# Optimization experiments

Measured on AMD Instinct MI355X. Metric: run time of the kernel, lower is better.

Reference implementation:

```python
import jax, jax.numpy as jnp
import numpy as np

B, T, D = 2, 2048, 1024
NH, NKV, HD = 16, 4, 64
ROPE = 16  # partial RoPE dims (first 16 of 64)
HALF = ROPE // 2


def apply_rope(x, cos, sin):
    # x: (B, nH, T, HD); rotate first ROPE dims, pass the rest through
    x1 = x[..., :HALF]
    x2 = x[..., HALF:ROPE]
    xp = x[..., ROPE:]
    c = cos[None, None, :, :]  # (1,1,T,HALF)
    s = sin[None, None, :, :]
    return jnp.concatenate([x1 * c - x2 * s, x1 * s + x2 * c, xp], axis=-1)


def setup_inputs() -> dict:
    key = jax.random.key(0)
    k0, k1, k2 = jax.random.split(key, 3)
    x = jax.random.normal(k0, (B, T, D), dtype=jnp.float32)
    # RoPE tables for the rotated sub-dimension (half = ROPE//2 = 8)
    inv_freq = 1.0 / (10000.0 ** (jnp.arange(HALF, dtype=jnp.float32) / HALF))
    ang = jnp.arange(T, dtype=jnp.float32)[:, None] * inv_freq[None, :]
    cos = jnp.cos(ang)
    sin = jnp.sin(ang)
    attn_mask = jnp.tril(jnp.ones((T, T), dtype=bool))  # causal
    w_qkv = jax.random.normal(k1, ((NH + 2 * NKV) * HD, D), dtype=jnp.float32) * (D ** -0.5)
    w_out = jax.random.normal(k2, (D, D), dtype=jnp.float32) * (D ** -0.5)
    q_scale = jnp.full((NH, 1), 1.5, dtype=jnp.float32)
    k_scale = jnp.full((NKV, 1), 1.5, dtype=jnp.float32)
    return {"x": x, "cos": cos, "sin": sin, "attn_mask": attn_mask,
            "w_qkv": w_qkv, "w_out": w_out, "q_scale": q_scale, "k_scale": k_scale}


def reference(x, cos, sin, attn_mask, w_qkv, w_out, q_scale, k_scale):
    Bx, Tx, C = x.shape
    groups = NH // NKV
    qkv = x @ w_qkv.T  # (B,T,(NH+2*NKV)*HD)
    q, k, v = jnp.split(qkv, [NH * HD, (NH + NKV) * HD], axis=-1)
    q = q.reshape(Bx, Tx, NH, HD).transpose(0, 2, 1, 3)    # (B,NH,T,HD)
    k = k.reshape(Bx, Tx, NKV, HD).transpose(0, 2, 1, 3)   # (B,NKV,T,HD)
    v = v.reshape(Bx, Tx, NKV, HD).transpose(0, 2, 1, 3)
    # per-head qk gain scaling
    q = q * q_scale[None, :, :, None]  # (1,NH,1,1)
    k = k * k_scale[None, :, :, None]
    # partial RoPE on q and k
    q = apply_rope(q, cos[:Tx], sin[:Tx])
    k = apply_rope(k, cos[:Tx], sin[:Tx])
    # GQA expand (repeat_interleave along heads)
    ke = jnp.repeat(k, groups, axis=1)  # (B,NH,T,HD)
    ve = jnp.repeat(v, groups, axis=1)
    # scaled dot-product attention with causal mask
    scores = jnp.einsum('bhqd,bhkd->bhqk', q, ke) * (HD ** -0.5)
    scores = jnp.where(attn_mask[None, None], scores, -jnp.inf)
    probs = jax.nn.softmax(scores, axis=-1)
    ao = jnp.einsum('bhqk,bhkd->bhqd', probs, ve)  # (B,NH,T,HD)
    # xsa: subtract self-component along the (shared) kv value direction
    ao_r = ao.reshape(Bx, NKV, groups, Tx, HD)
    vv = v[:, :, None]  # (B,NKV,1,T,HD), broadcasts over groups
    dots = jnp.sum(ao_r * vv, axis=-1, keepdims=True)
    norm = jnp.maximum(jnp.sum(vv * vv, axis=-1, keepdims=True), 1e-8)
    ao = (ao_r - (dots / norm) * vv).reshape(Bx, NH, Tx, HD)
    out = ao.transpose(0, 2, 1, 3).reshape(Bx, Tx, C) @ w_out.T
    return out
```

## Files before the change

### kernel.cpp

```cpp
#include <hip/hip_runtime.h>
#include <hip/hip_bf16.h>

#define NB 2
#define NT 2048
#define ND 1024
#define NHEADS 16
#define NKVH 4
#define HDIM 64
#define QKVD 1536

typedef __attribute__((ext_vector_type(8))) short short8;
typedef __attribute__((ext_vector_type(4))) float floatx4;

#if defined(__has_builtin)
#  if __has_builtin(__builtin_amdgcn_global_load_lds)
#    define HAS_GLL 1
#  endif
#endif
#ifndef HAS_GLL
#  define HAS_GLL 0
#endif

__device__ __forceinline__ void gll16(const void* g, void* l, int lane) {
#if HAS_GLL
  (void)lane;
  __builtin_amdgcn_global_load_lds(
      (const __attribute__((address_space(1))) unsigned int*)g,
      (__attribute__((address_space(3))) unsigned int*)l, 16, 0, 0);
#else
  *(short8*)((short*)l) = *(const short8*)g;
#endif
}

__device__ __forceinline__ unsigned short f2bf(float f) {
  union { float f; unsigned int u; } cv; cv.f = f;
  unsigned int u = cv.u;
  u += 0x7fffu + ((u >> 16) & 1u);
  return (unsigned short)(u >> 16);
}
__device__ __forceinline__ float bf2f(unsigned short u) {
  union { unsigned int u; float f; } cv; cv.u = ((unsigned int)u) << 16; return cv.f;
}

#define N4_X   1048576
#define N4_WQ   393216
#define N4_WO   262144
__global__ __launch_bounds__(256) void cvt_all(
    const float* __restrict__ x, const float* __restrict__ wq,
    const float* __restrict__ wo,
    unsigned short* __restrict__ xb, unsigned short* __restrict__ wqb,
    unsigned short* __restrict__ wob) {
  int i = blockIdx.x * 256 + threadIdx.x;
  const float* src; unsigned short* dst; int j;
  if (i < N4_X)              { src = x;  dst = xb;  j = i; }
  else if (i < N4_X + N4_WQ) { src = wq; dst = wqb; j = i - N4_X; }
  else                       { src = wo; dst = wob; j = i - N4_X - N4_WQ; }
  float4 v = ((const float4*)src)[j];
  ushort4 o;
  o.x = f2bf(v.x); o.y = f2bf(v.y); o.z = f2bf(v.z); o.w = f2bf(v.w);
  ((ushort4*)dst)[j] = o;
}

#define GEMM4W_PROLOGUE(Aptr, Bptr, Kdim)                                      \
  __shared__ __align__(16) short As[2][128][32];                               \
  __shared__ __align__(16) short Bs[2][128][32];                               \
  const int tid = threadIdx.x;                                                 \
  const int wid = tid >> 6;                                                    \
  const int wr = wid >> 1, wc = wid & 1;                                       \
  const int lane = tid & 63;                                                   \
  const int quad = lane >> 4, l16 = lane & 15;                                 \
  const int srow = tid >> 2;                                                   \
  const int sch  = ((tid & 3) ^ (srow & 3)) * 8;                               \
  const unsigned short* agp = (Aptr) + (size_t)(m0 + srow) * (Kdim) + sch;     \
  const unsigned short* bgp = (Bptr) + (size_t)(n0 + srow) * (Kdim) + sch;     \
  short* asb = &As[0][0][0];                                                   \
  short* bsb = &Bs[0][0][0];                                                   \
  const int lofs = (HAS_GLL ? wid * 512 : tid * 8);                            \
  const int cs = (quad ^ (l16 & 3)) * 8;                                       \
  floatx4 acc[4][4] = {};                                                      \
  _Pragma("unroll")                                                            \
  for (int g = 0; g < 2; g++) {                                                \
    gll16(agp + (size_t)(64 * g) * (Kdim), asb + g * 2048 + lofs, lane);       \
    gll16(bgp + (size_t)(64 * g) * (Kdim), bsb + g * 2048 + lofs, lane);       \
  }                                                                            \
  const int NIT = (Kdim) / 32;                                                 \
  for (int it = 0; it < NIT; it++) {                                           \
    __syncthreads();                                                           \
    const int bi = it & 1, bn = bi ^ 1;                                        \
    if (it + 1 < NIT) {                                                        \
      const int k = (it + 1) * 32;                                             \
      _Pragma("unroll")                                                        \
      for (int g = 0; g < 2; g++) {                                            \
        gll16(agp + (size_t)(64 * g) * (Kdim) + k, asb + bn * 4096 + g * 2048 + lofs, lane); \
        gll16(bgp + (size_t)(64 * g) * (Kdim) + k, bsb + bn * 4096 + g * 2048 + lofs, lane); \
      }                                                                        \
    }                                                                          \
    short8 af[4], bf[4];                                                       \
    _Pragma("unroll")                                                          \
    for (int mi = 0; mi < 4; mi++)                                             \
      af[mi] = *(const short8*)(asb + bi * 4096 + (wr * 64 + mi * 16 + l16) * 32 + cs); \
    _Pragma("unroll")                                                          \
    for (int ni = 0; ni < 4; ni++)                                             \
      bf[ni] = *(const short8*)(bsb + bi * 4096 + (wc * 64 + ni * 16 + l16) * 32 + cs); \
    _Pragma("unroll")                                                          \
    for (int mi = 0; mi < 4; mi++)                                             \
      _Pragma("unroll")                                                        \
      for (int ni = 0; ni < 4; ni++)                                           \
        acc[mi][ni] = __builtin_amdgcn_mfma_f32_16x16x32_bf16(af[mi], bf[ni], acc[mi][ni], 0, 0, 0); \
  }

__global__ __launch_bounds__(256) void gemm_qkv(
    const unsigned short* __restrict__ A,
    const unsigned short* __restrict__ Bm,
    const float* __restrict__ cosT, const float* __restrict__ sinT,
    const float* __restrict__ q_scale, const float* __restrict__ k_scale,
    unsigned short* __restrict__ qb, unsigned short* __restrict__ kb,
    unsigned short* __restrict__ vtb)
{
  const int m0 = blockIdx.x * 128, n0 = blockIdx.y * 128;
  GEMM4W_PROLOGUE(A, Bm, ND)

  const int hh = blockIdx.y * 2 + wc;
  const int mw0 = m0 + wr * 64;
  const int lo8 = l16 & 7;

  if (hh >= NHEADS + NKVH) {
    const int kvh = hh - (NHEADS + NKVH);
#pragma unroll
    for (int mi = 0; mi < 4; mi++) {
      const int mrow = mw0 + mi * 16 + quad * 4;
      const int bb = mrow >> 11, tt = mrow & (NT - 1);
#pragma unroll
      for (int ni = 0; ni < 4; ni++) {
        const int d = ni * 16 + l16;
        ushort4 w;
        w.x = f2bf(acc[mi][ni][0]); w.y = f2bf(acc[mi][ni][1]);
        w.z = f2bf(acc[mi][ni][2]); w.w = f2bf(acc[mi][ni][3]);
        *(ushort4*)(vtb + ((size_t)((bb * NKVH + kvh) * HDIM + d)) * NT + tt) = w;
      }
    }
  } else {
    float scl; unsigned short* dst0; int hloc, nh;
    if (hh < NHEADS) { scl = q_scale[hh] * (0.125f * 1.44269504088896f); hloc = hh; dst0 = qb; nh = NHEADS; }
    else             { scl = k_scale[hh - NHEADS]; hloc = hh - NHEADS; dst0 = kb; nh = NKVH; }
#pragma unroll
    for (int mi = 0; mi < 4; mi++) {
#pragma unroll
      for (int r = 0; r < 4; r++) {
        const int mrow = mw0 + mi * 16 + quad * 4 + r;
        const int bb = mrow >> 11, tt = mrow & (NT - 1);
        unsigned short* drow = dst0 + ((size_t)((bb * nh + hloc) * NT + tt)) * HDIM;

        const float own = acc[mi][0][r];
        const float oth = __shfl_xor(own, 8);
        const float c = cosT[tt * 8 + lo8], s = sinT[tt * 8 + lo8];
        const float roped = (l16 < 8) ? (own * c - oth * s)
                                      : (oth * s + own * c);
        drow[l16] = f2bf(roped * scl);
#pragma unroll
        for (int ni = 1; ni < 4; ni++)
          drow[ni * 16 + l16] = f2bf(acc[mi][ni][r] * scl);
      }
    }
  }
}

__global__ __launch_bounds__(256) void gemm_out(
    const unsigned short* __restrict__ A,
    const unsigned short* __restrict__ Bm,
    float* __restrict__ C, int M, int N, int K)
{
  const int m0 = blockIdx.x * 128, n0 = blockIdx.y * 128;
  GEMM4W_PROLOGUE(A, Bm, K)

#pragma unroll
  for (int mi = 0; mi < 4; mi++)
#pragma unroll
    for (int ni = 0; ni < 4; ni++)
#pragma unroll
      for (int r = 0; r < 4; r++) {
        int m = m0 + wr * 64 + mi * 16 + quad * 4 + r;
        int n = n0 + wc * 64 + ni * 16 + l16;
        C[(size_t)m * N + n] = acc[mi][ni][r];
      }
}

__global__ __launch_bounds__(256) void fattn(
    const unsigned short* __restrict__ qb,
    const unsigned short* __restrict__ kb,
    const unsigned short* __restrict__ vtb,
    unsigned short* __restrict__ aob,
    float* __restrict__ pbuf)
{
  const int idx = blockIdx.x;
  const int h = blockIdx.y, b = blockIdx.z;
  const int kv = h >> 2;

  int qt, j0, cnt, chunk; bool direct;
  if (idx < 16) { qt = 16 + idx; j0 = 0; cnt = 16; chunk = 0; direct = false; }
  else {
    int rel = idx - 16, s = 16 - (rel >> 1);
    if ((rel & 1) == 0) { qt = s - 1;  j0 = 0;  cnt = s; chunk = 0; direct = true;  }
    else                { qt = s + 15; j0 = 16; cnt = s; chunk = 1; direct = false; }
  }

  const int tid = threadIdx.x;
  const int wid = tid >> 6, lane = tid & 63;
  const int quad = lane >> 4, l16 = lane & 15;
  const int lo8 = l16 & 7;

  __shared__ __align__(16) short Ks[2][64][64];
  __shared__ __align__(16) short Vs[2][64][64];
  __shared__ __align__(16) short Ps[4][16][64];

  const unsigned short* qg = qb + ((size_t)((b * NHEADS + h) * NT + qt * 64)) * HDIM;
  const int qrow = wid * 16 + l16;
  short8 aq0 = *(const short8*)(qg + (size_t)qrow * HDIM + quad * 8);
  short8 aq1 = *(const short8*)(qg + (size_t)qrow * HDIM + 32 + quad * 8);

  const int sr  = tid >> 3;
  const int lck = ((tid & 7) ^ (sr & 7)) * 8;
  const unsigned short* kgp0 = kb  + ((size_t)((b * NKVH + kv) * NT) + sr) * HDIM + lck;
  const unsigned short* vgp0 = vtb + ((size_t)((b * NKVH + kv) * HDIM) + sr) * NT + lck;
  short* ksb = &Ks[0][0][0];
  short* vsb = &Vs[0][0][0];
  const int lofs = (HAS_GLL ? wid * 512 : tid * 8);

  const int cs0 = (quad ^ lo8) * 8;
  const int cs1 = cs0 ^ 32;

  char* psb = (char*)&Ps[0][0][0];
  int psw[4];
#pragma unroll
  for (int nb = 0; nb < 4; nb++)
    psw[nb] = wid * 2048 + l16 * 128 +
              ((((nb << 1) | (quad >> 1)) ^ lo8) << 4) + ((quad & 1) << 3);
  const int pr0 = wid * 2048 + l16 * 128 + ((quad ^ lo8) << 4);

  floatx4 acc_o[4] = {};
  float lsum = 0.f;

  {
    const unsigned short* kg = kgp0 + (size_t)j0 * 64 * HDIM;
    const unsigned short* vg = vgp0 + j0 * 64;
    gll16(kg, ksb + lofs, lane);
    gll16(kg + 32 * HDIM, ksb + 2048 + lofs, lane);
    gll16(vg, vsb + lofs, lane);
    gll16(vg + (size_t)32 * NT, vsb + 2048 + lofs, lane);
  }

  for (int i = 0; i < cnt; i++) {
    const int jt = j0 + i;
    __syncthreads();
    const int bi = i & 1, bn = bi ^ 1;
    if (i + 1 < cnt) {
      const unsigned short* kg = kgp0 + (size_t)(jt + 1) * 64 * HDIM;
      const unsigned short* vg = vgp0 + (jt + 1) * 64;
      gll16(kg, ksb + bn * 4096 + lofs, lane);
      gll16(kg + 32 * HDIM, ksb + bn * 4096 + 2048 + lofs, lane);
      gll16(vg, vsb + bn * 4096 + lofs, lane);
      gll16(vg + (size_t)32 * NT, vsb + bn * 4096 + 2048 + lofs, lane);
    }

    floatx4 s[4] = {};
#pragma unroll
    for (int nb = 0; nb < 4; nb++) {
      short8 bk0 = *(const short8*)&Ks[bi][nb * 16 + l16][cs0];
      short8 bk1 = *(const short8*)&Ks[bi][nb * 16 + l16][cs1];
      s[nb] = __builtin_amdgcn_mfma_f32_16x16x32_bf16(bk0, aq0, s[nb], 0, 0, 0);
      s[nb] = __builtin_amdgcn_mfma_f32_16x16x32_bf16(bk1, aq1, s[nb], 0, 0, 0);
    }

    if (jt == qt) {
      const int qloc = wid * 16 + l16;
#pragma unroll
      for (int nb = 0; nb < 4; nb++)
#pragma unroll
        for (int r = 0; r < 4; r++)
          if (nb * 16 + quad * 4 + r > qloc) s[nb][r] = -INFINITY;
    }

#pragma unroll
    for (int nb = 0; nb < 4; nb++) {
      float p0 = __builtin_amdgcn_exp2f(s[nb][0]);
      float p1 = __builtin_amdgcn_exp2f(s[nb][1]);
      float p2 = __builtin_amdgcn_exp2f(s[nb][2]);
      float p3 = __builtin_amdgcn_exp2f(s[nb][3]);
      lsum += (p0 + p1) + (p2 + p3);
      unsigned int pk0, pk1;
      asm("v_cvt_pk_bf16_f32 %0, %1, %2" : "=v"(pk0) : "v"(p0), "v"(p1));
      asm("v_cvt_pk_bf16_f32 %0, %1, %2" : "=v"(pk1) : "v"(p2), "v"(p3));
      uint2 w; w.x = pk0; w.y = pk1;
      *(uint2*)(psb + psw[nb]) = w;
    }

    short8 ap0 = *(const short8*)(psb + pr0);
    short8 ap1 = *(const short8*)(psb + (pr0 ^ 64));
#pragma unroll
    for (int nb = 0; nb < 4; nb++) {
      short8 bv0 = *(const short8*)&Vs[bi][nb * 16 + l16][cs0];
      short8 bv1 = *(const short8*)&Vs[bi][nb * 16 + l16][cs1];
      acc_o[nb] = __builtin_amdgcn_mfma_f32_16x16x32_bf16(ap0, bv0, acc_o[nb], 0, 0, 0);
      acc_o[nb] = __builtin_amdgcn_mfma_f32_16x16x32_bf16(ap1, bv1, acc_o[nb], 0, 0, 0);
    }
  }

  const int bl = (cnt - 1) & 1;

  float lst = lsum;
  lst += __shfl_xor(lst, 16);
  lst += __shfl_xor(lst, 32);

  if (direct) {
#pragma unroll
    for (int r = 0; r < 4; r++) {
      const int rowl = wid * 16 + quad * 4 + r;
      const float invl = 1.f / __shfl(lst, quad * 4 + r);

      const int vcol = ((rowl >> 3) ^ lo8) * 8 + (rowl & 7);
      float vd[4], dot = 0.f, vv = 0.f;
#pragma unroll
      for (int nb = 0; nb < 4; nb++) {
        vd[nb] = bf2f((unsigned short)Vs[bl][nb * 16 + l16][vcol]);
        dot += acc_o[nb][r] * invl * vd[nb];
        vv  += vd[nb] * vd[nb];
      }
#pragma unroll
      for (int off = 1; off < 16; off <<= 1) {
        dot += __shfl_xor(dot, off);
        vv  += __shfl_xor(vv, off);
      }
      const float coef = dot / fmaxf(vv, 1e-8f);
      unsigned short* dst = aob + ((size_t)(b * NT + qt * 64 + rowl)) * ND + h * HDIM + l16;
#pragma unroll
      for (int nb = 0; nb < 4; nb++)
        dst[nb * 16] = f2bf(acc_o[nb][r] * invl - coef * vd[nb]);
    }
  } else {
    const int slot = ((b * NHEADS + h) * 16 + (qt - 16)) * 2 + chunk;
    float* pO = pbuf + (size_t)slot * 4160;
    float* pl = pO + 4096;
    if (quad == 0) pl[wid * 16 + l16] = lst;
#pragma unroll
    for (int r = 0; r < 4; r++) {
      const int rowl = wid * 16 + quad * 4 + r;
#pragma unroll
      for (int nb = 0; nb < 4; nb++)
        pO[rowl * 64 + nb * 16 + l16] = acc_o[nb][r];
    }
  }
}

__global__ __launch_bounds__(256) void redn(
    const float* __restrict__ pbuf,
    const unsigned short* __restrict__ vtb,
    unsigned short* __restrict__ aob)
{
  const int qt = 16 + blockIdx.x;
  const int h = blockIdx.y, b = blockIdx.z;
  const int kv = h >> 2;
  const int tid = threadIdx.x;

  const int slot0 = ((b * NHEADS + h) * 16 + blockIdx.x) * 2;
  const float* O0 = pbuf + (size_t)slot0 * 4160;
  const float* O1 = O0 + 4160;
  const float* l0 = O0 + 4096;
  const float* l1 = O1 + 4096;

  __shared__ short vt[64][66];

  {
    const int d = tid >> 2, tq = (tid & 3) * 16;
    const unsigned short* src = vtb + ((size_t)((b * NKVH + kv) * HDIM + d)) * NT + qt * 64 + tq;
    short8 v0 = *(const short8*)src;
    short8 v1 = *(const short8*)(src + 8);
    *(short8*)&vt[d][tq] = v0;
    *(short8*)&vt[d][tq + 8] = v1;
  }
  __syncthreads();

  const int row = tid >> 2, dq = tid & 3;
  const float invl = 1.f / (l0[row] + l1[row]);

  float o[16], vd[16];
  float dot = 0.f, vv = 0.f;
#pragma unroll
  for (int j = 0; j < 16; j++) {
    const int d = dq * 16 + j;
    float ov = (O0[row * 64 + d] + O1[row * 64 + d]) * invl;
    float v  = bf2f((unsigned short)vt[d][row]);
    o[j] = ov; vd[j] = v;
    dot += ov * v; vv += v * v;
  }
  dot += __shfl_xor(dot, 1); dot += __shfl_xor(dot, 2);
  vv  += __shfl_xor(vv, 1);  vv  += __shfl_xor(vv, 2);
  const float coef = dot / fmaxf(vv, 1e-8f);

  unsigned short* dst = aob + ((size_t)(b * NT + qt * 64 + row)) * ND + h * HDIM + dq * 16;
  ushort4 w0, w1, w2, w3;
  w0.x = f2bf(o[0] - coef * vd[0]);  w0.y = f2bf(o[1] - coef * vd[1]);
  w0.z = f2bf(o[2] - coef * vd[2]);  w0.w = f2bf(o[3] - coef * vd[3]);
  w1.x = f2bf(o[4] - coef * vd[4]);  w1.y = f2bf(o[5] - coef * vd[5]);
  w1.z = f2bf(o[6] - coef * vd[6]);  w1.w = f2bf(o[7] - coef * vd[7]);
  w2.x = f2bf(o[8] - coef * vd[8]);  w2.y = f2bf(o[9] - coef * vd[9]);
  w2.z = f2bf(o[10] - coef * vd[10]); w2.w = f2bf(o[11] - coef * vd[11]);
  w3.x = f2bf(o[12] - coef * vd[12]); w3.y = f2bf(o[13] - coef * vd[13]);
  w3.z = f2bf(o[14] - coef * vd[14]); w3.w = f2bf(o[15] - coef * vd[15]);
  ((ushort4*)dst)[0] = w0; ((ushort4*)dst)[1] = w1;
  ((ushort4*)dst)[2] = w2; ((ushort4*)dst)[3] = w3;
}

extern "C" void kernel_launch(void* const* d_in, const int* in_sizes, int n_in,
                              void* d_out, int out_size, void* d_ws, size_t ws_size,
                              hipStream_t stream) {
  const float* x       = (const float*)d_in[0];
  const float* cosT    = (const float*)d_in[1];
  const float* sinT    = (const float*)d_in[2];
  const float* w_qkv   = (const float*)d_in[4];
  const float* w_out   = (const float*)d_in[5];
  const float* q_scale = (const float*)d_in[6];
  const float* k_scale = (const float*)d_in[7];
  float* out = (float*)d_out;

  char* ws = (char*)d_ws;
  unsigned short* xb    = (unsigned short*)ws;
  unsigned short* wqkvb = (unsigned short*)(ws + 8388608);
  float*          pbuf  = (float*)ws;
  unsigned short* woutb = (unsigned short*)(ws + 17825792);
  unsigned short* qb    = (unsigned short*)(ws + 19922944);
  unsigned short* kb    = (unsigned short*)(ws + 28311552);
  unsigned short* vtb   = (unsigned short*)(ws + 30408704);
  unsigned short* aob   = (unsigned short*)(ws + 32505856);

  cvt_all<<<(N4_X + N4_WQ + N4_WO) / 256, 256, 0, stream>>>(
      x, w_qkv, w_out, xb, wqkvb, woutb);

  gemm_qkv<<<dim3(NB * NT / 128, QKVD / 128), 256, 0, stream>>>(
      xb, wqkvb, cosT, sinT, q_scale, k_scale, qb, kb, vtb);

  fattn<<<dim3(48, NHEADS, NB), 256, 0, stream>>>(qb, kb, vtb, aob, pbuf);
  redn<<<dim3(16, NHEADS, NB), 256, 0, stream>>>(pbuf, vtb, aob);

  gemm_out<<<dim3(NB * NT / 128, ND / 128), 256, 0, stream>>>(
      aob, woutb, out, NB * NT, ND, ND);
}
```

Before: 191.9 us.

## Quadruple-buffer K/V tiles and sync every two attention iterations

The K/V shared-memory staging grows from two to four buffers. The prologue preloads the first two tiles, and the loop now issues prefetches for tiles i+2 and i+3 behind a single barrier taken on even iterations. This halves the number of block barriers and gives async loads more lead time. The cost is doubled K/V LDS usage, which may lower the number of resident blocks per CU.

```diff
diff --git a/kernel.cpp b/kernel.cpp
--- a/kernel.cpp
+++ b/kernel.cpp
@@ -209,8 +209,8 @@
   const int quad = lane >> 4, l16 = lane & 15;
   const int lo8 = l16 & 7;
 
-  __shared__ __align__(16) short Ks[2][64][64];
-  __shared__ __align__(16) short Vs[2][64][64];
+  __shared__ __align__(16) short Ks[4][64][64];
+  __shared__ __align__(16) short Vs[4][64][64];
   __shared__ __align__(16) short Ps[4][16][64];
 
   const unsigned short* qg = qb + ((size_t)((b * NHEADS + h) * NT + qt * 64)) * HDIM;
@@ -247,19 +247,39 @@
     gll16(kg + 32 * HDIM, ksb + 2048 + lofs, lane);
     gll16(vg, vsb + lofs, lane);
     gll16(vg + (size_t)32 * NT, vsb + 2048 + lofs, lane);
+    if (cnt > 1) {
+      const unsigned short* kg1 = kgp0 + (size_t)(j0 + 1) * 64 * HDIM;
+      const unsigned short* vg1 = vgp0 + (j0 + 1) * 64;
+      gll16(kg1, ksb + 4096 + lofs, lane);
+      gll16(kg1 + 32 * HDIM, ksb + 4096 + 2048 + lofs, lane);
+      gll16(vg1, vsb + 4096 + lofs, lane);
+      gll16(vg1 + (size_t)32 * NT, vsb + 4096 + 2048 + lofs, lane);
+    }
   }
 
   for (int i = 0; i < cnt; i++) {
     const int jt = j0 + i;
-    __syncthreads();
-    const int bi = i & 1, bn = bi ^ 1;
-    if (i + 1 < cnt) {
-      const unsigned short* kg = kgp0 + (size_t)(jt + 1) * 64 * HDIM;
-      const unsigned short* vg = vgp0 + (jt + 1) * 64;
-      gll16(kg, ksb + bn * 4096 + lofs, lane);
-      gll16(kg + 32 * HDIM, ksb + bn * 4096 + 2048 + lofs, lane);
-      gll16(vg, vsb + bn * 4096 + lofs, lane);
-      gll16(vg + (size_t)32 * NT, vsb + bn * 4096 + 2048 + lofs, lane);
+    const int bi = i & 3;
+    if ((i & 1) == 0) {
+      __syncthreads();
+      if (i + 2 < cnt) {
+        const int b2 = (i + 2) & 3;
+        const unsigned short* kg = kgp0 + (size_t)(jt + 2) * 64 * HDIM;
+        const unsigned short* vg = vgp0 + (jt + 2) * 64;
+        gll16(kg, ksb + b2 * 4096 + lofs, lane);
+        gll16(kg + 32 * HDIM, ksb + b2 * 4096 + 2048 + lofs, lane);
+        gll16(vg, vsb + b2 * 4096 + lofs, lane);
+        gll16(vg + (size_t)32 * NT, vsb + b2 * 4096 + 2048 + lofs, lane);
+      }
+      if (i + 3 < cnt) {
+        const int b3 = (i + 3) & 3;
+        const unsigned short* kg = kgp0 + (size_t)(jt + 3) * 64 * HDIM;
+        const unsigned short* vg = vgp0 + (jt + 3) * 64;
+        gll16(kg, ksb + b3 * 4096 + lofs, lane);
+        gll16(kg + 32 * HDIM, ksb + b3 * 4096 + 2048 + lofs, lane);
+        gll16(vg, vsb + b3 * 4096 + lofs, lane);
+        gll16(vg + (size_t)32 * NT, vsb + b3 * 4096 + 2048 + lofs, lane);
+      }
     }
 
     floatx4 s[4] = {};
@@ -305,7 +325,7 @@
     }
   }
 
-  const int bl = (cnt - 1) & 1;
+  const int bl = (cnt - 1) & 3;
 
   float lst = lsum;
   lst += __shfl_xor(lst, 16);
```

New measurement: 199.3 us. 3.9% more time.

## Drop split-KV attention and reduction kernel; one block per query tile, longest first

Applied to the files above, without the earlier changes.

Replaces the split-KV scheme, which split the upper query tiles into two chunks with a float partial buffer and a separate reduction kernel, with a plain one-block-per-query-tile causal attention launch. Tiles are ordered heaviest first to balance the triangular workload. This removes the partial-buffer round trip and one kernel launch. In exchange the per-block work becomes more uneven (up to 32 KV tiles) and there are fewer blocks, which can lengthen the tail.

```diff
diff --git a/kernel.cpp b/kernel.cpp
--- a/kernel.cpp
+++ b/kernel.cpp
@@ -189,20 +189,12 @@
     const unsigned short* __restrict__ qb,
     const unsigned short* __restrict__ kb,
     const unsigned short* __restrict__ vtb,
-    unsigned short* __restrict__ aob,
-    float* __restrict__ pbuf)
+    unsigned short* __restrict__ aob)
 {
-  const int idx = blockIdx.x;
+  const int qt = (NT / 64 - 1) - blockIdx.x;
   const int h = blockIdx.y, b = blockIdx.z;
   const int kv = h >> 2;
-
-  int qt, j0, cnt, chunk; bool direct;
-  if (idx < 16) { qt = 16 + idx; j0 = 0; cnt = 16; chunk = 0; direct = false; }
-  else {
-    int rel = idx - 16, s = 16 - (rel >> 1);
-    if ((rel & 1) == 0) { qt = s - 1;  j0 = 0;  cnt = s; chunk = 0; direct = true;  }
-    else                { qt = s + 15; j0 = 16; cnt = s; chunk = 1; direct = false; }
-  }
+  const int cnt = qt + 1;
 
   const int tid = threadIdx.x;
   const int wid = tid >> 6, lane = tid & 63;
@@ -241,8 +233,8 @@
   float lsum = 0.f;
 
   {
-    const unsigned short* kg = kgp0 + (size_t)j0 * 64 * HDIM;
-    const unsigned short* vg = vgp0 + j0 * 64;
+    const unsigned short* kg = kgp0;
+    const unsigned short* vg = vgp0;
     gll16(kg, ksb + lofs, lane);
     gll16(kg + 32 * HDIM, ksb + 2048 + lofs, lane);
     gll16(vg, vsb + lofs, lane);
@@ -250,7 +242,7 @@
   }
 
   for (int i = 0; i < cnt; i++) {
-    const int jt = j0 + i;
+    const int jt = i;
     __syncthreads();
     const int bi = i & 1, bn = bi ^ 1;
     if (i + 1 < cnt) {
@@ -311,103 +303,30 @@
   lst += __shfl_xor(lst, 16);
   lst += __shfl_xor(lst, 32);
 
-  if (direct) {
-#pragma unroll
-    for (int r = 0; r < 4; r++) {
-      const int rowl = wid * 16 + quad * 4 + r;
-      const float invl = 1.f / __shfl(lst, quad * 4 + r);
-
-      const int vcol = ((rowl >> 3) ^ lo8) * 8 + (rowl & 7);
-      float vd[4], dot = 0.f, vv = 0.f;
-#pragma unroll
-      for (int nb = 0; nb < 4; nb++) {
-        vd[nb] = bf2f((unsigned short)Vs[bl][nb * 16 + l16][vcol]);
-        dot += acc_o[nb][r] * invl * vd[nb];
-        vv  += vd[nb] * vd[nb];
-      }
-#pragma unroll
-      for (int off = 1; off < 16; off <<= 1) {
-        dot += __shfl_xor(dot, off);
-        vv  += __shfl_xor(vv, off);
-      }
-      const float coef = dot / fmaxf(vv, 1e-8f);
-      unsigned short* dst = aob + ((size_t)(b * NT + qt * 64 + rowl)) * ND + h * HDIM + l16;
-#pragma unroll
-      for (int nb = 0; nb < 4; nb++)
-        dst[nb * 16] = f2bf(acc_o[nb][r] * invl - coef * vd[nb]);
-    }
-  } else {
-    const int slot = ((b * NHEADS + h) * 16 + (qt - 16)) * 2 + chunk;
-    float* pO = pbuf + (size_t)slot * 4160;
-    float* pl = pO + 4096;
-    if (quad == 0) pl[wid * 16 + l16] = lst;
-#pragma unroll
-    for (int r = 0; r < 4; r++) {
-      const int rowl = wid * 16 + quad * 4 + r;
-#pragma unroll
-      for (int nb = 0; nb < 4; nb++)
-        pO[rowl * 64 + nb * 16 + l16] = acc_o[nb][r];
-    }
-  }
-}
-
-__global__ __launch_bounds__(256) void redn(
-    const float* __restrict__ pbuf,
-    const unsigned short* __restrict__ vtb,
-    unsigned short* __restrict__ aob)
-{
-  const int qt = 16 + blockIdx.x;
-  const int h = blockIdx.y, b = blockIdx.z;
-  const int kv = h >> 2;
-  const int tid = threadIdx.x;
-
-  const int slot0 = ((b * NHEADS + h) * 16 + blockIdx.x) * 2;
-  const float* O0 = pbuf + (size_t)slot0 * 4160;
-  const float* O1 = O0 + 4160;
-  const float* l0 = O0 + 4096;
-  const float* l1 = O1 + 4096;
-
-  __shared__ short vt[64][66];
-
-  {
-    const int d = tid >> 2, tq = (tid & 3) * 16;
-    const unsigned short* src = vtb + ((size_t)((b * NKVH + kv) * HDIM + d)) * NT + qt * 64 + tq;
-    short8 v0 = *(const short8*)src;
-    short8 v1 = *(const short8*)(src + 8);
-    *(short8*)&vt[d][tq] = v0;
-    *(short8*)&vt[d][tq + 8] = v1;
-  }
-  __syncthreads();
-
-  const int row = tid >> 2, dq = tid & 3;
-  const float invl = 1.f / (l0[row] + l1[row]);
-
-  float o[16], vd[16];
-  float dot = 0.f, vv = 0.f;
-#pragma unroll
-  for (int j = 0; j < 16; j++) {
-    const int d = dq * 16 + j;
-    float ov = (O0[row * 64 + d] + O1[row * 64 + d]) * invl;
-    float v  = bf2f((unsigned short)vt[d][row]);
-    o[j] = ov; vd[j] = v;
-    dot += ov * v; vv += v * v;
-  }
-  dot += __shfl_xor(dot, 1); dot += __shfl_xor(dot, 2);
-  vv  += __shfl_xor(vv, 1);  vv  += __shfl_xor(vv, 2);
-  const float coef = dot / fmaxf(vv, 1e-8f);
-
-  unsigned short* dst = aob + ((size_t)(b * NT + qt * 64 + row)) * ND + h * HDIM + dq * 16;
-  ushort4 w0, w1, w2, w3;
-  w0.x = f2bf(o[0] - coef * vd[0]);  w0.y = f2bf(o[1] - coef * vd[1]);
-  w0.z = f2bf(o[2] - coef * vd[2]);  w0.w = f2bf(o[3] - coef * vd[3]);
-  w1.x = f2bf(o[4] - coef * vd[4]);  w1.y = f2bf(o[5] - coef * vd[5]);
-  w1.z = f2bf(o[6] - coef * vd[6]);  w1.w = f2bf(o[7] - coef * vd[7]);
-  w2.x = f2bf(o[8] - coef * vd[8]);  w2.y = f2bf(o[9] - coef * vd[9]);
-  w2.z = f2bf(o[10] - coef * vd[10]); w2.w = f2bf(o[11] - coef * vd[11]);
-  w3.x = f2bf(o[12] - coef * vd[12]); w3.y = f2bf(o[13] - coef * vd[13]);
-  w3.z = f2bf(o[14] - coef * vd[14]); w3.w = f2bf(o[15] - coef * vd[15]);
-  ((ushort4*)dst)[0] = w0; ((ushort4*)dst)[1] = w1;
-  ((ushort4*)dst)[2] = w2; ((ushort4*)dst)[3] = w3;
+#pragma unroll
+  for (int r = 0; r < 4; r++) {
+    const int rowl = wid * 16 + quad * 4 + r;
+    const float invl = 1.f / __shfl(lst, quad * 4 + r);
+
+    const int vcol = ((rowl >> 3) ^ lo8) * 8 + (rowl & 7);
+    float vd[4], dot = 0.f, vv = 0.f;
+#pragma unroll
+    for (int nb = 0; nb < 4; nb++) {
+      vd[nb] = bf2f((unsigned short)Vs[bl][nb * 16 + l16][vcol]);
+      dot += acc_o[nb][r] * invl * vd[nb];
+      vv  += vd[nb] * vd[nb];
+    }
+#pragma unroll
+    for (int off = 1; off < 16; off <<= 1) {
+      dot += __shfl_xor(dot, off);
+      vv  += __shfl_xor(vv, off);
+    }
+    const float coef = dot / fmaxf(vv, 1e-8f);
+    unsigned short* dst = aob + ((size_t)(b * NT + qt * 64 + rowl)) * ND + h * HDIM + l16;
+#pragma unroll
+    for (int nb = 0; nb < 4; nb++)
+      dst[nb * 16] = f2bf(acc_o[nb][r] * invl - coef * vd[nb]);
+  }
 }
 
 extern "C" void kernel_launch(void* const* d_in, const int* in_sizes, int n_in,
@@ -425,7 +344,6 @@
   char* ws = (char*)d_ws;
   unsigned short* xb    = (unsigned short*)ws;
   unsigned short* wqkvb = (unsigned short*)(ws + 8388608);
-  float*          pbuf  = (float*)ws;
   unsigned short* woutb = (unsigned short*)(ws + 17825792);
   unsigned short* qb    = (unsigned short*)(ws + 19922944);
   unsigned short* kb    = (unsigned short*)(ws + 28311552);
@@ -438,8 +356,7 @@
   gemm_qkv<<<dim3(NB * NT / 128, QKVD / 128), 256, 0, stream>>>(
       xb, wqkvb, cosT, sinT, q_scale, k_scale, qb, kb, vtb);
 
-  fattn<<<dim3(48, NHEADS, NB), 256, 0, stream>>>(qb, kb, vtb, aob, pbuf);
-  redn<<<dim3(16, NHEADS, NB), 256, 0, stream>>>(pbuf, vtb, aob);
+  fattn<<<dim3(NT / 64, NHEADS, NB), 256, 0, stream>>>(qb, kb, vtb, aob);
 
   gemm_out<<<dim3(NB * NT / 128, ND / 128), 256, 0, stream>>>(
       aob, woutb, out, NB * NT, ND, ND);
```

Result: slower. 197.7 us (+3.0%).
